# Kernel optimization log

Measured on AMD Instinct MI355X. Metric: run time of the kernel, lower is better.

Reference implementation:

```python
import jax, jax.numpy as jnp
import numpy as np

B, L, C, H, RATIO = 2, 512, 256, 8, 4
D = C // H
EPS = 1e-5


def layernorm(x, g, b):
    m = jnp.mean(x, axis=-1, keepdims=True)
    v = jnp.mean((x - m) ** 2, axis=-1, keepdims=True)
    return (x - m) * jax.lax.rsqrt(v + EPS) * g + b


def setup_inputs() -> dict:
    key = jax.random.key(0)
    ks = jax.random.split(key, 10)
    s = 0.02
    return {
        "x": jax.random.normal(ks[0], (B, L, C), jnp.float32),
        "relative_pos": jax.random.normal(ks[1], (B, L, L, C), jnp.float32),
        # attention params (qkv_bias=False)
        "w_qkv": jax.random.normal(ks[2], (C, 3 * C), jnp.float32) * s,
        "w_proj": jax.random.normal(ks[3], (C, C), jnp.float32) * s,
        "b_proj": jnp.zeros((C,), jnp.float32),
        # relative_project: Linear(C,H) -> GELU -> LayerNorm(H)
        "w_rel": jax.random.normal(ks[4], (C, H), jnp.float32) * s,
        "b_rel": jnp.zeros((H,), jnp.float32),
        "g_reln": jnp.ones((H,), jnp.float32),
        "b_reln": jnp.zeros((H,), jnp.float32),
        # block layernorms
        "g_n1": jnp.ones((C,), jnp.float32),
        "b_n1": jnp.zeros((C,), jnp.float32),
        "g_n2": jnp.ones((C,), jnp.float32),
        "b_n2": jnp.zeros((C,), jnp.float32),
        # MLP (mlp_ratio=4, act=GELU)
        "w_mlp1": jax.random.normal(ks[5], (C, RATIO * C), jnp.float32) * s,
        "b_mlp1": jnp.zeros((RATIO * C,), jnp.float32),
        "w_mlp2": jax.random.normal(ks[6], (RATIO * C, C), jnp.float32) * s,
        "b_mlp2": jnp.zeros((C,), jnp.float32),
    }


def reference(x, relative_pos, w_qkv, w_proj, b_proj, w_rel, b_rel,
              g_reln, b_reln, g_n1, b_n1, g_n2, b_n2,
              w_mlp1, b_mlp1, w_mlp2, b_mlp2):
    # eval mode: dropout / droppath are identity
    scale = D ** -0.5

    # --- attention branch ---
    h = layernorm(x, g_n1, b_n1)                      # [B,L,C]
    qkv = (h @ w_qkv).reshape(B, L, 3, H, D)
    qkv = jnp.transpose(qkv, (2, 0, 3, 1, 4))          # [3,B,H,L,D]
    q, k, v = qkv[0], qkv[1], qkv[2]

    attn = jnp.einsum("bhid,bhjd->bhij", q, k)        # [B,H,L,L]

    # relative bias: Linear -> GELU(exact) -> LayerNorm over heads
    rel = jax.nn.gelu(relative_pos @ w_rel + b_rel, approximate=False)  # [B,L,L,H]
    rel = layernorm(rel, g_reln, b_reln)
    rel = jnp.transpose(rel, (0, 3, 1, 2))            # [B,H,L,L]

    attn = jax.nn.softmax((attn + rel) * scale, axis=-1)
    o = jnp.einsum("bhij,bhjd->bhid", attn, v)        # [B,H,L,D]
    o = jnp.transpose(o, (0, 2, 1, 3)).reshape(B, L, C)
    o = o @ w_proj + b_proj
    x = x + o

    # --- MLP branch (jump=False since out_feat==in_feat) ---
    h = layernorm(x, g_n2, b_n2)
    h = jax.nn.gelu(h @ w_mlp1 + b_mlp1, approximate=False)
    h = h @ w_mlp2 + b_mlp2
    return x + h
```

## Files before the change

kernel.cpp:

```cpp
#include <hip/hip_runtime.h>
#include <cstddef>

#define EPS_ 1e-5f
#define SCALE_ 0.1767766952966369f

typedef short bf16x8_t __attribute__((ext_vector_type(8)));
typedef float f32x4_t  __attribute__((ext_vector_type(4)));

__device__ __forceinline__ float gelu_f(float x) {
    return 0.5f * x * (1.0f + erff(x * 0.7071067811865476f));
}
__device__ __forceinline__ unsigned short f2bf(float f) {
    unsigned u = __builtin_bit_cast(unsigned, f);
    u += 0x7FFFu + ((u >> 16) & 1u);
    return (unsigned short)(u >> 16);
}

__global__ __launch_bounds__(256) void ln_kernel(const float* __restrict__ x,
                                                 const float* __restrict__ g,
                                                 const float* __restrict__ b,
                                                 unsigned short* __restrict__ out) {
    int wid = threadIdx.x >> 6, lane = threadIdx.x & 63;
    int row = blockIdx.x * 4 + wid;
    const float4 xv = *(const float4*)(x + (size_t)row * 256 + lane * 4);
    float s  = xv.x + xv.y + xv.z + xv.w;
    float sq = xv.x*xv.x + xv.y*xv.y + xv.z*xv.z + xv.w*xv.w;
#pragma unroll
    for (int m = 1; m < 64; m <<= 1) { s += __shfl_xor(s, m); sq += __shfl_xor(sq, m); }
    float mean = s * (1.0f/256.0f);
    float var  = sq * (1.0f/256.0f) - mean*mean;
    float rstd = rsqrtf(var + EPS_);
    float4 gv = *(const float4*)(g + lane*4);
    float4 bv = *(const float4*)(b + lane*4);
    ushort4 o;
    o.x = f2bf((xv.x-mean)*rstd*gv.x + bv.x);
    o.y = f2bf((xv.y-mean)*rstd*gv.y + bv.y);
    o.z = f2bf((xv.z-mean)*rstd*gv.z + bv.z);
    o.w = f2bf((xv.w-mean)*rstd*gv.w + bv.w);
    *(ushort4*)(out + (size_t)row * 256 + lane * 4) = o;
}

__global__ __launch_bounds__(256) void convw_kernel(
    const float* __restrict__ w_qkv,  unsigned short* __restrict__ wqkvT,
    const float* __restrict__ w_proj, unsigned short* __restrict__ wprojT,
    const float* __restrict__ w_mlp1, unsigned short* __restrict__ wmlp1T,
    const float* __restrict__ w_mlp2, unsigned short* __restrict__ wmlp2T) {
    __shared__ float tile[32][33];
    int bid = blockIdx.x, t = threadIdx.x;
    const float* W; unsigned short* WT; int K, N, tt;
    if (bid < 192)      { W = w_qkv;  WT = wqkvT;  K = 256;  N = 768;  tt = bid; }
    else if (bid < 256) { W = w_proj; WT = wprojT; K = 256;  N = 256;  tt = bid - 192; }
    else if (bid < 512) { W = w_mlp1; WT = wmlp1T; K = 256;  N = 1024; tt = bid - 256; }
    else                { W = w_mlp2; WT = wmlp2T; K = 1024; N = 256;  tt = bid - 512; }
    int ntn = N >> 5;
    int kt = tt / ntn, nt = tt % ntn;
    int k0 = kt * 32, n0 = nt * 32;
    {
        int kr = t >> 3, cg = (t & 7) * 4;
        float4 v = *(const float4*)(W + (size_t)(k0 + kr) * N + n0 + cg);
        tile[kr][cg+0] = v.x; tile[kr][cg+1] = v.y; tile[kr][cg+2] = v.z; tile[kr][cg+3] = v.w;
    }
    __syncthreads();
    {
        int nr = t >> 3, kg = (t & 7) * 4;
        ushort4 o;
        o.x = f2bf(tile[kg+0][nr]); o.y = f2bf(tile[kg+1][nr]);
        o.z = f2bf(tile[kg+2][nr]); o.w = f2bf(tile[kg+3][nr]);
        *(ushort4*)(WT + (size_t)(n0 + nr) * K + k0 + kg) = o;
    }
}

template<bool BIAS, bool GACT, bool RESID, bool BF16OUT, int KSPLIT>
__global__ __launch_bounds__(256) void mgemm_kernel(
    const unsigned short* __restrict__ A, const unsigned short* __restrict__ BT,
    const float* __restrict__ bias, const float* __restrict__ resid,
    void* __restrict__ Cout, int M, int N, int K) {
    __shared__ unsigned short Al[64][40];
    __shared__ unsigned short Bl[64][40];
    int t = threadIdx.x;
    int bm = blockIdx.x, bn = blockIdx.y, kz = blockIdx.z;
    int kchunk = K / KSPLIT;
    int srow = t >> 2, skk = (t & 3) * 8;
    const unsigned short* Ap = A  + (size_t)(bm*64 + srow) * K + kz*kchunk + skk;
    const unsigned short* Bp = BT + (size_t)(bn*64 + srow) * K + kz*kchunk + skk;
    int lane = t & 63, w = t >> 6, wr = w >> 1, wc = w & 1;
    int fr = lane & 15, fg = lane >> 4;
    f32x4_t a00 = {0.f,0.f,0.f,0.f}, a01 = {0.f,0.f,0.f,0.f};
    f32x4_t a10 = {0.f,0.f,0.f,0.f}, a11 = {0.f,0.f,0.f,0.f};
    for (int kk = 0; kk < kchunk; kk += 32) {
        uint4 av = *(const uint4*)(Ap + kk);
        uint4 bv = *(const uint4*)(Bp + kk);
        __syncthreads();
        *(uint4*)&Al[srow][skk] = av;
        *(uint4*)&Bl[srow][skk] = bv;
        __syncthreads();
        bf16x8_t fa0 = *(const bf16x8_t*)&Al[wr*32      + fr][fg*8];
        bf16x8_t fa1 = *(const bf16x8_t*)&Al[wr*32 + 16 + fr][fg*8];
        bf16x8_t fb0 = *(const bf16x8_t*)&Bl[wc*32      + fr][fg*8];
        bf16x8_t fb1 = *(const bf16x8_t*)&Bl[wc*32 + 16 + fr][fg*8];
        a00 = __builtin_amdgcn_mfma_f32_16x16x32_bf16(fa0, fb0, a00, 0, 0, 0);
        a01 = __builtin_amdgcn_mfma_f32_16x16x32_bf16(fa0, fb1, a01, 0, 0, 0);
        a10 = __builtin_amdgcn_mfma_f32_16x16x32_bf16(fa1, fb0, a10, 0, 0, 0);
        a11 = __builtin_amdgcn_mfma_f32_16x16x32_bf16(fa1, fb1, a11, 0, 0, 0);
    }
    float* Cf = (float*)Cout + (KSPLIT > 1 ? (size_t)kz * M * N : (size_t)0);
    unsigned short* Cb = (unsigned short*)Cout;
    auto emit = [&](f32x4_t acc, int mi, int ni) {
        int Ro = bm*64 + wr*32 + mi*16 + fg*4;
        int Co = bn*64 + wc*32 + ni*16 + fr;
        float bval = BIAS ? bias[Co] : 0.f;
#pragma unroll
        for (int e = 0; e < 4; ++e) {
            int r = Ro + e;
            float v = acc[e];
            if (BIAS)  v += bval;
            if (GACT)  v = gelu_f(v);
            if (RESID) v += resid[(size_t)r * N + Co];
            if (BF16OUT) Cb[(size_t)r * N + Co] = f2bf(v);
            else         Cf[(size_t)r * N + Co] = v;
        }
    };
    emit(a00, 0, 0); emit(a01, 0, 1); emit(a10, 1, 0); emit(a11, 1, 1);
}

__global__ __launch_bounds__(256) void qk_kernel(const float* __restrict__ qkv,
                                                 float* __restrict__ qk) {
    __shared__ float k_lds[512*32];
    int t = threadIdx.x;
    int it = blockIdx.x;
    int h  = blockIdx.y;
    int b  = blockIdx.z;
    const float* base = qkv + (size_t)b * 393216;
#pragma unroll
    for (int r = 0; r < 16; ++r) {
        int idx = r*256 + t;
        int row = idx >> 3, c4 = idx & 7;
        float4 kv = *(const float4*)(base + (size_t)row*768 + 256 + h*32 + c4*4);
        *(float4*)(k_lds + row*32 + c4*4) = kv;
    }
    __syncthreads();
    int ir = t & 31, jg = t >> 5;
    int i = it*32 + ir;
    float4 q[8];
    const float* qp = base + (size_t)i*768 + h*32;
#pragma unroll
    for (int c4 = 0; c4 < 8; ++c4) q[c4] = *(const float4*)(qp + c4*4);
    float* outp = qk + (((size_t)(b*512 + i))*8 + h)*512 + jg*64;
    for (int jj = 0; jj < 64; jj += 4) {
        float a4[4];
#pragma unroll
        for (int u = 0; u < 4; ++u) {
            const float* kp = k_lds + (size_t)(jg*64 + jj + u)*32;
            float acc = 0.f;
#pragma unroll
            for (int c4 = 0; c4 < 8; ++c4) {
                float4 kv = *(const float4*)(kp + c4*4);
                acc += q[c4].x*kv.x + q[c4].y*kv.y + q[c4].z*kv.z + q[c4].w*kv.w;
            }
            a4[u] = acc;
        }
        *(float4*)(outp + jj) = make_float4(a4[0], a4[1], a4[2], a4[3]);
    }
}

#define LGS 520
__global__ __launch_bounds__(256) void rel_softmax_kernel(
    const float* __restrict__ rp, const float* __restrict__ qk,
    const float* __restrict__ w_rel, const float* __restrict__ b_rel,
    const float* __restrict__ g_reln, const float* __restrict__ b_reln,
    float* __restrict__ attn) {
    __shared__ float lg_lds[8*LGS];
    int t = threadIdx.x;
    int bi = blockIdx.x;
    int wid = t >> 6, lane = t & 63;
    int fr = lane & 15, fg = lane >> 4;
    bool act = fr < 8;
    bf16x8_t bfrag[8];
#pragma unroll
    for (int kk = 0; kk < 8; ++kk) {
        bf16x8_t bf;
#pragma unroll
        for (int e = 0; e < 8; ++e) {
            float v = act ? w_rel[(size_t)(kk*32 + fg*8 + e)*8 + fr] : 0.f;
            bf[e] = (short)f2bf(v);
        }
        bfrag[kk] = bf;
    }
    float brel = act ? b_rel[fr]  : 0.f;
    float grn  = act ? g_reln[fr] : 1.f;
    float brn  = act ? b_reln[fr] : 0.f;
    const float* rpb = rp + (size_t)bi * 512 * 256;
#pragma unroll 1
    for (int tile = 0; tile < 8; ++tile) {
        int j0 = wid*128 + tile*16;
        const float* arow = rpb + (size_t)(j0 + fr)*256 + fg*8;
        f32x4_t acc = {0.f,0.f,0.f,0.f};
#pragma unroll
        for (int kk = 0; kk < 8; ++kk) {
            float4 x0 = *(const float4*)(arow + kk*32);
            float4 x1 = *(const float4*)(arow + kk*32 + 4);
            bf16x8_t af;
            af[0] = (short)f2bf(x0.x); af[1] = (short)f2bf(x0.y);
            af[2] = (short)f2bf(x0.z); af[3] = (short)f2bf(x0.w);
            af[4] = (short)f2bf(x1.x); af[5] = (short)f2bf(x1.y);
            af[6] = (short)f2bf(x1.z); af[7] = (short)f2bf(x1.w);
            acc = __builtin_amdgcn_mfma_f32_16x16x32_bf16(af, bfrag[kk], acc, 0, 0, 0);
        }
#pragma unroll
        for (int r = 0; r < 4; ++r) {
            float val = acc[r] + brel;
            float gv = 0.5f * val * (1.0f + erff(val * 0.7071067811865476f));
            float sm = gv, sq = gv*gv;
            sm += __shfl_xor(sm, 1); sq += __shfl_xor(sq, 1);
            sm += __shfl_xor(sm, 2); sq += __shfl_xor(sq, 2);
            sm += __shfl_xor(sm, 4); sq += __shfl_xor(sq, 4);
            float mean = sm * 0.125f;
            float var  = sq * 0.125f - mean*mean;
            float reln = (gv - mean) * rsqrtf(var + EPS_) * grn + brn;
            if (act) lg_lds[fr*LGS + j0 + fg*4 + r] = reln;
        }
    }
    __syncthreads();
    {
        int h = wid*2 + (lane >> 5);
        int sub = lane & 31;
        float* row = lg_lds + h*LGS + sub*16;
        const float* qrow = qk + ((size_t)bi*8 + h)*512 + sub*16;
        float v[16];
        float4 q0 = *(const float4*)(qrow + 0),  q1 = *(const float4*)(qrow + 4);
        float4 q2 = *(const float4*)(qrow + 8),  q3 = *(const float4*)(qrow + 12);
        float4 r0 = *(float4*)(row + 0),  r1 = *(float4*)(row + 4);
        float4 r2 = *(float4*)(row + 8),  r3 = *(float4*)(row + 12);
        v[0]=(q0.x+r0.x)*SCALE_; v[1]=(q0.y+r0.y)*SCALE_; v[2]=(q0.z+r0.z)*SCALE_; v[3]=(q0.w+r0.w)*SCALE_;
        v[4]=(q1.x+r1.x)*SCALE_; v[5]=(q1.y+r1.y)*SCALE_; v[6]=(q1.z+r1.z)*SCALE_; v[7]=(q1.w+r1.w)*SCALE_;
        v[8]=(q2.x+r2.x)*SCALE_; v[9]=(q2.y+r2.y)*SCALE_; v[10]=(q2.z+r2.z)*SCALE_; v[11]=(q2.w+r2.w)*SCALE_;
        v[12]=(q3.x+r3.x)*SCALE_; v[13]=(q3.y+r3.y)*SCALE_; v[14]=(q3.z+r3.z)*SCALE_; v[15]=(q3.w+r3.w)*SCALE_;
        float mx = v[0];
#pragma unroll
        for (int e = 1; e < 16; ++e) mx = fmaxf(mx, v[e]);
#pragma unroll
        for (int m = 1; m < 32; m <<= 1) mx = fmaxf(mx, __shfl_xor(mx, m));
        float s = 0.f;
#pragma unroll
        for (int e = 0; e < 16; ++e) { v[e] = expf(v[e] - mx); s += v[e]; }
#pragma unroll
        for (int m = 1; m < 32; m <<= 1) s += __shfl_xor(s, m);
        float inv = 1.0f / s;
#pragma unroll
        for (int e = 0; e < 16; ++e) v[e] *= inv;
        float* dst = attn + (size_t)bi*4096 + h*512 + sub*16;
        *(float4*)(dst +  0) = *(float4*)(v +  0);
        *(float4*)(dst +  4) = *(float4*)(v +  4);
        *(float4*)(dst +  8) = *(float4*)(v +  8);
        *(float4*)(dst + 12) = *(float4*)(v + 12);
    }
}

__global__ __launch_bounds__(256) void attnv_kernel(const float* __restrict__ attn,
                                                    const float* __restrict__ qkv,
                                                    unsigned short* __restrict__ o) {
    __shared__ float a_lds[4*8*512];
    int t = threadIdx.x;
    int bi0 = blockIdx.x * 4;
    int b = bi0 >> 9;
    const float4* asrc = (const float4*)(attn + (size_t)bi0*4096);
    float4* adst = (float4*)a_lds;
#pragma unroll
    for (int r = 0; r < 16; ++r) adst[r*256 + t] = asrc[r*256 + t];
    __syncthreads();
    int c = t, h = c >> 5;
    const float* vcol = qkv + (size_t)b*393216 + 512 + c;
    float acc0 = 0.f, acc1 = 0.f, acc2 = 0.f, acc3 = 0.f;
    for (int j = 0; j < 512; j += 2) {
        float vv0 = vcol[(size_t)j*768];
        float vv1 = vcol[(size_t)(j+1)*768];
        acc0 += a_lds[(0*8+h)*512 + j]*vv0 + a_lds[(0*8+h)*512 + j+1]*vv1;
        acc1 += a_lds[(1*8+h)*512 + j]*vv0 + a_lds[(1*8+h)*512 + j+1]*vv1;
        acc2 += a_lds[(2*8+h)*512 + j]*vv0 + a_lds[(2*8+h)*512 + j+1]*vv1;
        acc3 += a_lds[(3*8+h)*512 + j]*vv0 + a_lds[(3*8+h)*512 + j+1]*vv1;
    }
    o[(size_t)(bi0+0)*256 + c] = f2bf(acc0);
    o[(size_t)(bi0+1)*256 + c] = f2bf(acc1);
    o[(size_t)(bi0+2)*256 + c] = f2bf(acc2);
    o[(size_t)(bi0+3)*256 + c] = f2bf(acc3);
}

__global__ __launch_bounds__(256) void combine_kernel(const float* __restrict__ part,
                                                      const float* __restrict__ bias,
                                                      const float* __restrict__ resid,
                                                      float* __restrict__ out) {
    int f = blockIdx.x * 256 + threadIdx.x;
    int e = f * 4;
    float4 r  = *(const float4*)(resid + e);
    float4 bv = *(const float4*)(bias + (e & 255));
    float4 p0 = *(const float4*)(part + e);
    float4 p1 = *(const float4*)(part + 262144 + e);
    float4 p2 = *(const float4*)(part + 524288 + e);
    float4 p3 = *(const float4*)(part + 786432 + e);
    float4 o4;
    o4.x = r.x + bv.x + p0.x + p1.x + p2.x + p3.x;
    o4.y = r.y + bv.y + p0.y + p1.y + p2.y + p3.y;
    o4.z = r.z + bv.z + p0.z + p1.z + p2.z + p3.z;
    o4.w = r.w + bv.w + p0.w + p1.w + p2.w + p3.w;
    *(float4*)(out + e) = o4;
}

extern "C" void kernel_launch(void* const* d_in, const int* in_sizes, int n_in,
                              void* d_out, int out_size, void* d_ws, size_t ws_size,
                              hipStream_t stream) {
    const float* x      = (const float*)d_in[0];
    const float* rp     = (const float*)d_in[1];
    const float* w_qkv  = (const float*)d_in[2];
    const float* w_proj = (const float*)d_in[3];
    const float* b_proj = (const float*)d_in[4];
    const float* w_rel  = (const float*)d_in[5];
    const float* b_rel  = (const float*)d_in[6];
    const float* g_reln = (const float*)d_in[7];
    const float* b_reln = (const float*)d_in[8];
    const float* g_n1   = (const float*)d_in[9];
    const float* b_n1   = (const float*)d_in[10];
    const float* g_n2   = (const float*)d_in[11];
    const float* b_n2   = (const float*)d_in[12];
    const float* w_mlp1 = (const float*)d_in[13];
    const float* b_mlp1 = (const float*)d_in[14];
    const float* w_mlp2 = (const float*)d_in[15];
    const float* b_mlp2 = (const float*)d_in[16];
    float* out = (float*)d_out;

    float* ws      = (float*)d_ws;
    float* ws_qkv  = ws;
    float* ws_qk   = ws_qkv + 786432;
    float* ws_attn = ws_qk  + 4194304;
    float* ws_x1   = ws_attn + 4194304;
    float* ws_pt   = ws_x1  + 262144;
    unsigned short* ub = (unsigned short*)(ws_pt + 1048576);
    unsigned short* hbf    = ub;
    unsigned short* obf    = hbf  + 262144;
    unsigned short* h2bf   = obf  + 262144;
    unsigned short* hgbf   = h2bf + 262144;
    unsigned short* wqkvT  = hgbf + 1048576;
    unsigned short* wprojT = wqkvT + 196608;
    unsigned short* wmlp1T = wprojT + 65536;
    unsigned short* wmlp2T = wmlp1T + 262144;

    convw_kernel<<<768, 256, 0, stream>>>(w_qkv, wqkvT, w_proj, wprojT,
                                          w_mlp1, wmlp1T, w_mlp2, wmlp2T);
    ln_kernel<<<256, 256, 0, stream>>>(x, g_n1, b_n1, hbf);
    mgemm_kernel<false,false,false,false,1><<<dim3(16,12,1), 256, 0, stream>>>(
        hbf, wqkvT, nullptr, nullptr, ws_qkv, 1024, 768, 256);
    qk_kernel<<<dim3(16,8,2), 256, 0, stream>>>(ws_qkv, ws_qk);
    rel_softmax_kernel<<<1024, 256, 0, stream>>>(rp, ws_qk, w_rel, b_rel, g_reln, b_reln, ws_attn);
    attnv_kernel<<<256, 256, 0, stream>>>(ws_attn, ws_qkv, obf);
    mgemm_kernel<true,false,true,false,1><<<dim3(16,4,1), 256, 0, stream>>>(
        obf, wprojT, b_proj, x, ws_x1, 1024, 256, 256);
    ln_kernel<<<256, 256, 0, stream>>>(ws_x1, g_n2, b_n2, h2bf);
    mgemm_kernel<true,true,false,true,1><<<dim3(16,16,1), 256, 0, stream>>>(
        h2bf, wmlp1T, b_mlp1, nullptr, hgbf, 1024, 1024, 256);
    mgemm_kernel<false,false,false,false,4><<<dim3(16,4,4), 256, 0, stream>>>(
        hgbf, wmlp2T, nullptr, nullptr, ws_pt, 1024, 256, 1024);
    combine_kernel<<<256, 256, 0, stream>>>(ws_pt, b_mlp2, ws_x1, out);
}
```

Measured before the change: 223.0 us.

## Store attention in bf16, use fast gelu/exp and packed bf16 conversions

The softmax output matrix is now written as bf16 instead of fp32 and converted back to fp32 when loaded into LDS in the attn·V kernel, halving that intermediate's traffic. The exact erf GELU is replaced by a tanh approximation built from __expf and rcp, softmax uses __expf, and the bf16 conversions use the HIP intrinsic with packed two-per-word stores. Softmax loads and stores are reorganised so lanes access contiguous float4 chunks. The tanh GELU departs from the reference's exact GELU and the bf16 attention adds rounding error, which risks tolerance failures.

Measured after the change: 222.9 us. No clear change (-0.1%).

```diff
diff --git a/kernel.cpp b/kernel.cpp
--- a/kernel.cpp
+++ b/kernel.cpp
@@ -1,4 +1,5 @@
 #include <hip/hip_runtime.h>
+#include <hip/hip_bf16.h>
 #include <cstddef>
 
 #define EPS_ 1e-5f
@@ -8,12 +9,22 @@
 typedef float f32x4_t  __attribute__((ext_vector_type(4)));
 
 __device__ __forceinline__ float gelu_f(float x) {
-    return 0.5f * x * (1.0f + erff(x * 0.7071067811865476f));
+    float y = 0.7978845608028654f * (x + 0.044715f * x * x * x);
+    float e = __expf(2.0f * y);
+    float t = 1.0f - 2.0f * __builtin_amdgcn_rcpf(e + 1.0f);
+    return 0.5f * x * (1.0f + t);
 }
 __device__ __forceinline__ unsigned short f2bf(float f) {
-    unsigned u = __builtin_bit_cast(unsigned, f);
-    u += 0x7FFFu + ((u >> 16) & 1u);
-    return (unsigned short)(u >> 16);
+    return __builtin_bit_cast(unsigned short, __float2bfloat16(f));
+}
+__device__ __forceinline__ unsigned f2bf2(float a, float b) {
+    unsigned lo = __builtin_bit_cast(unsigned short, __float2bfloat16(a));
+    unsigned hi = __builtin_bit_cast(unsigned short, __float2bfloat16(b));
+    return lo | (hi << 16);
+}
+__device__ __forceinline__ float bf2f(unsigned short s) {
+    unsigned u = (unsigned)s << 16;
+    return __builtin_bit_cast(float, u);
 }
 
 __global__ __launch_bounds__(256) void ln_kernel(const float* __restrict__ x,
@@ -32,12 +43,10 @@
     float rstd = rsqrtf(var + EPS_);
     float4 gv = *(const float4*)(g + lane*4);
     float4 bv = *(const float4*)(b + lane*4);
-    ushort4 o;
-    o.x = f2bf((xv.x-mean)*rstd*gv.x + bv.x);
-    o.y = f2bf((xv.y-mean)*rstd*gv.y + bv.y);
-    o.z = f2bf((xv.z-mean)*rstd*gv.z + bv.z);
-    o.w = f2bf((xv.w-mean)*rstd*gv.w + bv.w);
-    *(ushort4*)(out + (size_t)row * 256 + lane * 4) = o;
+    uint2 o;
+    o.x = f2bf2((xv.x-mean)*rstd*gv.x + bv.x, (xv.y-mean)*rstd*gv.y + bv.y);
+    o.y = f2bf2((xv.z-mean)*rstd*gv.z + bv.z, (xv.w-mean)*rstd*gv.w + bv.w);
+    *(uint2*)(out + (size_t)row * 256 + lane * 4) = o;
 }
 
 __global__ __launch_bounds__(256) void convw_kernel(
@@ -63,10 +72,10 @@
     __syncthreads();
     {
         int nr = t >> 3, kg = (t & 7) * 4;
-        ushort4 o;
-        o.x = f2bf(tile[kg+0][nr]); o.y = f2bf(tile[kg+1][nr]);
-        o.z = f2bf(tile[kg+2][nr]); o.w = f2bf(tile[kg+3][nr]);
-        *(ushort4*)(WT + (size_t)(n0 + nr) * K + k0 + kg) = o;
+        uint2 o;
+        o.x = f2bf2(tile[kg+0][nr], tile[kg+1][nr]);
+        o.y = f2bf2(tile[kg+2][nr], tile[kg+3][nr]);
+        *(uint2*)(WT + (size_t)(n0 + nr) * K + k0 + kg) = o;
     }
 }
 
@@ -168,7 +177,7 @@
     const float* __restrict__ rp, const float* __restrict__ qk,
     const float* __restrict__ w_rel, const float* __restrict__ b_rel,
     const float* __restrict__ g_reln, const float* __restrict__ b_reln,
-    float* __restrict__ attn) {
+    unsigned short* __restrict__ attn) {
     __shared__ float lg_lds[8*LGS];
     int t = threadIdx.x;
     int bi = blockIdx.x;
@@ -199,17 +208,17 @@
         for (int kk = 0; kk < 8; ++kk) {
             float4 x0 = *(const float4*)(arow + kk*32);
             float4 x1 = *(const float4*)(arow + kk*32 + 4);
-            bf16x8_t af;
-            af[0] = (short)f2bf(x0.x); af[1] = (short)f2bf(x0.y);
-            af[2] = (short)f2bf(x0.z); af[3] = (short)f2bf(x0.w);
-            af[4] = (short)f2bf(x1.x); af[5] = (short)f2bf(x1.y);
-            af[6] = (short)f2bf(x1.z); af[7] = (short)f2bf(x1.w);
-            acc = __builtin_amdgcn_mfma_f32_16x16x32_bf16(af, bfrag[kk], acc, 0, 0, 0);
+            union { bf16x8_t v; uint4 u; } cvt;
+            cvt.u.x = f2bf2(x0.x, x0.y);
+            cvt.u.y = f2bf2(x0.z, x0.w);
+            cvt.u.z = f2bf2(x1.x, x1.y);
+            cvt.u.w = f2bf2(x1.z, x1.w);
+            acc = __builtin_amdgcn_mfma_f32_16x16x32_bf16(cvt.v, bfrag[kk], acc, 0, 0, 0);
         }
 #pragma unroll
         for (int r = 0; r < 4; ++r) {
             float val = acc[r] + brel;
-            float gv = 0.5f * val * (1.0f + erff(val * 0.7071067811865476f));
+            float gv = gelu_f(val);
             float sm = gv, sq = gv*gv;
             sm += __shfl_xor(sm, 1); sq += __shfl_xor(sq, 1);
             sm += __shfl_xor(sm, 2); sq += __shfl_xor(sq, 2);
@@ -224,17 +233,18 @@
     {
         int h = wid*2 + (lane >> 5);
         int sub = lane & 31;
-        float* row = lg_lds + h*LGS + sub*16;
-        const float* qrow = qk + ((size_t)bi*8 + h)*512 + sub*16;
+        const float* row  = lg_lds + h*LGS;
+        const float* qrow = qk + ((size_t)bi*8 + h)*512;
         float v[16];
-        float4 q0 = *(const float4*)(qrow + 0),  q1 = *(const float4*)(qrow + 4);
-        float4 q2 = *(const float4*)(qrow + 8),  q3 = *(const float4*)(qrow + 12);
-        float4 r0 = *(float4*)(row + 0),  r1 = *(float4*)(row + 4);
-        float4 r2 = *(float4*)(row + 8),  r3 = *(float4*)(row + 12);
-        v[0]=(q0.x+r0.x)*SCALE_; v[1]=(q0.y+r0.y)*SCALE_; v[2]=(q0.z+r0.z)*SCALE_; v[3]=(q0.w+r0.w)*SCALE_;
-        v[4]=(q1.x+r1.x)*SCALE_; v[5]=(q1.y+r1.y)*SCALE_; v[6]=(q1.z+r1.z)*SCALE_; v[7]=(q1.w+r1.w)*SCALE_;
-        v[8]=(q2.x+r2.x)*SCALE_; v[9]=(q2.y+r2.y)*SCALE_; v[10]=(q2.z+r2.z)*SCALE_; v[11]=(q2.w+r2.w)*SCALE_;
-        v[12]=(q3.x+r3.x)*SCALE_; v[13]=(q3.y+r3.y)*SCALE_; v[14]=(q3.z+r3.z)*SCALE_; v[15]=(q3.w+r3.w)*SCALE_;
+#pragma unroll
+        for (int c4 = 0; c4 < 4; ++c4) {
+            float4 r4 = *(const float4*)(row  + c4*128 + sub*4);
+            float4 q4 = *(const float4*)(qrow + c4*128 + sub*4);
+            v[c4*4+0] = (q4.x + r4.x) * SCALE_;
+            v[c4*4+1] = (q4.y + r4.y) * SCALE_;
+            v[c4*4+2] = (q4.z + r4.z) * SCALE_;
+            v[c4*4+3] = (q4.w + r4.w) * SCALE_;
+        }
         float mx = v[0];
 #pragma unroll
         for (int e = 1; e < 16; ++e) mx = fmaxf(mx, v[e]);
@@ -242,31 +252,37 @@
         for (int m = 1; m < 32; m <<= 1) mx = fmaxf(mx, __shfl_xor(mx, m));
         float s = 0.f;
 #pragma unroll
-        for (int e = 0; e < 16; ++e) { v[e] = expf(v[e] - mx); s += v[e]; }
+        for (int e = 0; e < 16; ++e) { v[e] = __expf(v[e] - mx); s += v[e]; }
 #pragma unroll
         for (int m = 1; m < 32; m <<= 1) s += __shfl_xor(s, m);
         float inv = 1.0f / s;
 #pragma unroll
         for (int e = 0; e < 16; ++e) v[e] *= inv;
-        float* dst = attn + (size_t)bi*4096 + h*512 + sub*16;
-        *(float4*)(dst +  0) = *(float4*)(v +  0);
-        *(float4*)(dst +  4) = *(float4*)(v +  4);
-        *(float4*)(dst +  8) = *(float4*)(v +  8);
-        *(float4*)(dst + 12) = *(float4*)(v + 12);
-    }
-}
-
-__global__ __launch_bounds__(256) void attnv_kernel(const float* __restrict__ attn,
+        unsigned short* dst = attn + (size_t)bi*4096 + h*512;
+#pragma unroll
+        for (int c4 = 0; c4 < 4; ++c4) {
+            uint2 o2;
+            o2.x = f2bf2(v[c4*4+0], v[c4*4+1]);
+            o2.y = f2bf2(v[c4*4+2], v[c4*4+3]);
+            *(uint2*)(dst + c4*128 + sub*4) = o2;
+        }
+    }
+}
+
+__global__ __launch_bounds__(256) void attnv_kernel(const unsigned short* __restrict__ attn,
                                                     const float* __restrict__ qkv,
                                                     unsigned short* __restrict__ o) {
     __shared__ float a_lds[4*8*512];
     int t = threadIdx.x;
     int bi0 = blockIdx.x * 4;
     int b = bi0 >> 9;
-    const float4* asrc = (const float4*)(attn + (size_t)bi0*4096);
-    float4* adst = (float4*)a_lds;
-#pragma unroll
-    for (int r = 0; r < 16; ++r) adst[r*256 + t] = asrc[r*256 + t];
+    const ushort4* asrc = (const ushort4*)(attn + (size_t)bi0*4096);
+#pragma unroll
+    for (int r = 0; r < 16; ++r) {
+        ushort4 s4 = asrc[r*256 + t];
+        float4 f4 = make_float4(bf2f(s4.x), bf2f(s4.y), bf2f(s4.z), bf2f(s4.w));
+        *(float4*)(a_lds + (size_t)(r*256 + t)*4) = f4;
+    }
     __syncthreads();
     int c = t, h = c >> 5;
     const float* vcol = qkv + (size_t)b*393216 + 512 + c;
@@ -330,11 +346,11 @@
     float* ws      = (float*)d_ws;
     float* ws_qkv  = ws;
     float* ws_qk   = ws_qkv + 786432;
-    float* ws_attn = ws_qk  + 4194304;
-    float* ws_x1   = ws_attn + 4194304;
+    float* ws_x1   = ws_qk  + 4194304;
     float* ws_pt   = ws_x1  + 262144;
     unsigned short* ub = (unsigned short*)(ws_pt + 1048576);
-    unsigned short* hbf    = ub;
+    unsigned short* attnbf = ub;
+    unsigned short* hbf    = attnbf + 4194304;
     unsigned short* obf    = hbf  + 262144;
     unsigned short* h2bf   = obf  + 262144;
     unsigned short* hgbf   = h2bf + 262144;
@@ -349,8 +365,8 @@
     mgemm_kernel<false,false,false,false,1><<<dim3(16,12,1), 256, 0, stream>>>(
         hbf, wqkvT, nullptr, nullptr, ws_qkv, 1024, 768, 256);
     qk_kernel<<<dim3(16,8,2), 256, 0, stream>>>(ws_qkv, ws_qk);
-    rel_softmax_kernel<<<1024, 256, 0, stream>>>(rp, ws_qk, w_rel, b_rel, g_reln, b_reln, ws_attn);
-    attnv_kernel<<<256, 256, 0, stream>>>(ws_attn, ws_qkv, obf);
+    rel_softmax_kernel<<<1024, 256, 0, stream>>>(rp, ws_qk, w_rel, b_rel, g_reln, b_reln, attnbf);
+    attnv_kernel<<<256, 256, 0, stream>>>(attnbf, ws_qkv, obf);
     mgemm_kernel<true,false,true,false,1><<<dim3(16,4,1), 256, 0, stream>>>(
         obf, wprojT, b_proj, x, ws_x1, 1024, 256, 256);
     ln_kernel<<<256, 256, 0, stream>>>(ws_x1, g_n2, b_n2, h2bf);
```
